# Kernel optimization log

Hardware: AMD Instinct MI355X
Metric: run time of the kernel (lower is better)

Reference implementation:

```python
import jax, jax.numpy as jnp
import numpy as np

E = 8          # moe_num_experts
F = 4096       # ffn_hidden_size
D = 2048       # d_model
TOP_K = 2


def setup_inputs() -> dict:
    key = jax.random.key(0)
    k_x, k_r, k_w1, k_v1, k_w2 = jax.random.split(key, 5)
    scale = 0.02  # ~ normal initializer scale
    x = jax.random.normal(k_x, (2, 2048, D), dtype=jnp.float32)
    router_w = jax.random.normal(k_r, (D, E), dtype=jnp.float32) * scale
    w1 = jax.random.normal(k_w1, (E * F, D), dtype=jnp.float32) * scale
    v1 = jax.random.normal(k_v1, (E * F, D), dtype=jnp.float32) * scale
    w2 = jax.random.normal(k_w2, (E * F, D), dtype=jnp.float32) * scale
    return {"x": x, "router_w": router_w, "w1": w1, "v1": v1, "w2": w2}


def reference(x, router_w, w1, v1, w2):
    # --- Router: dense logits -> softmax (fp32) -> top-k -> L1 normalize ---
    logits = jnp.einsum("bsd,de->bse", x.astype(jnp.float32), router_w)
    weights = jax.nn.softmax(logits, axis=-1)                       # [B,S,E]
    top_weights, top_experts = jax.lax.top_k(weights, TOP_K)        # [B,S,K]
    # moe_normalize_expert_weights = 1 -> L1 norm
    top_weights = top_weights / jnp.sum(jnp.abs(top_weights), axis=-1, keepdims=True)
    top_weights = top_weights.astype(x.dtype)

    # --- Experts: dense per-expert GLU, masked combine (faithful to source) ---
    w1r = w1.reshape(E, F, D)
    v1r = v1.reshape(E, F, D)
    w2r = w2.reshape(E, F, D)
    out = jnp.zeros_like(x)
    for e in range(E):  # fixed small structural loop over experts
        x1 = jnp.einsum("bsd,fd->bsf", x, w1r[e])
        x2 = jnp.einsum("bsd,fd->bsf", x, v1r[e])
        h = jax.nn.silu(x1) * x2                                    # GLU
        y = jnp.einsum("bsf,fd->bsd", h, w2r[e])
        coef = jnp.sum((top_experts == e) * top_weights, axis=-1)[:, :, None]
        out = out + coef * y
    return out
```

## Files before the change

kernel.cpp:

```cpp
#include <hip/hip_runtime.h>
#include <cstdio>
#include <cstdint>

typedef _Float16 f16;
typedef _Float16 f16x8 __attribute__((ext_vector_type(8)));
typedef float f32x4 __attribute__((ext_vector_type(4)));

#define D_MODEL 2048
#define FFN     4096
#define FFN2    8192
#define NEXP    8
#define NTOK    4096
#define NENT    (NTOK*2)
#define BM      256
#define BN      256
#define BK      64
#define KSPLIT  4
#define KCHUNK  (FFN / KSPLIT)
#define MAX_ROWS  10240
#define MAX_TILES 40

__device__ __forceinline__ void gload_lds16(const void* g, void* l) {
  __builtin_amdgcn_global_load_lds(
      (const __attribute__((address_space(1))) void*)g,
      (__attribute__((address_space(3))) void*)l, 16, 0, 0);
}

__device__ __forceinline__ void waitvm0() {
  asm volatile("s_waitcnt vmcnt(0)" ::: "memory");
}

template<int LD>
__device__ __forceinline__ void stageA(const f16* aT, int k0, f16* AS, int mh, int tid) {
#pragma unroll
  for (int s = 0; s < 2; s++) {
    int o = s*8192 + tid*16;
    int rl = o >> 7;
    int ce = ((o & 127) ^ ((rl & 7) << 4)) >> 1;
    int arow = s*128 + mh*64 + (rl & 63);
    gload_lds16(aT + (size_t)arow * LD + k0 + ce,
                (char*)AS + mh*16384 + s*8192 + (tid & ~63)*16);
  }
}

template<int LD>
__device__ __forceinline__ void stageB(const f16* bT, int k0, f16* BS, int nh, int tid) {
#pragma unroll
  for (int s = 0; s < 2; s++) {
    int o = s*8192 + tid*16;
    int rl = o >> 7;
    int ce = ((o & 127) ^ ((rl & 7) << 4)) >> 1;
    int crow = (rl >> 5)*64 + nh*32 + (rl & 31);
    gload_lds16(bT + (size_t)crow * LD + k0 + ce,
                (char*)BS + nh*16384 + s*8192 + (tid & ~63)*16);
  }
}

__device__ __forceinline__ f16x8 fragLd(const f16* S, int row, int lane, int ks) {
  int kb = ks*64 + (lane >> 4)*16;
  int off = (row*128 + kb) ^ ((row & 7) << 4);
  return *(const f16x8*)((const char*)S + off);
}

__device__ __forceinline__ void quad(
    f32x4 (&acc)[8][4], int mo, int no,
    f16x8 (&aF)[4][2], f16x8 (&bFh)[2][2]) {
#pragma unroll
  for (int mf = 0; mf < 4; mf++)
#pragma unroll
    for (int nf = 0; nf < 2; nf++)
#pragma unroll
      for (int ks = 0; ks < 2; ks++)
        acc[mo+mf][no+nf] = __builtin_amdgcn_mfma_f32_16x16x32_f16(
            aF[mf][ks], bFh[nf][ks], acc[mo+mf][no+nf], 0, 0, 0);
}

template<int LD, bool STG>
__device__ __forceinline__ void tileK2(
    const f16* aT, const f16* bT, int k1,
    const f16* ASc, const f16* BSc, f16* ASn, f16* BSn,
    f32x4 (&acc)[8][4], int tid, int lane, int wrM, int wcN) {
  if constexpr (STG) {
    stageA<LD>(aT, k1, ASn, 0, tid);
    stageA<LD>(aT, k1, ASn, 1, tid);
    stageB<LD>(bT, k1, BSn, 0, tid);
    stageB<LD>(bT, k1, BSn, 1, tid);
  }
  f16x8 aF[4][2], bF[2][2][2];
  int i15 = lane & 15;
#pragma unroll
  for (int mf = 0; mf < 4; mf++)
#pragma unroll
    for (int ks = 0; ks < 2; ks++)
      aF[mf][ks] = fragLd(ASc, wrM*64 + mf*16 + i15, lane, ks);
#pragma unroll
  for (int h = 0; h < 2; h++)
#pragma unroll
    for (int nf = 0; nf < 2; nf++)
#pragma unroll
      for (int ks = 0; ks < 2; ks++)
        bF[h][nf][ks] = fragLd(BSc, h*128 + wcN*32 + nf*16 + i15, lane, ks);
  quad(acc, 0, 0, aF, bF[0]);
  quad(acc, 0, 2, aF, bF[1]);
#pragma unroll
  for (int mf = 0; mf < 4; mf++)
#pragma unroll
    for (int ks = 0; ks < 2; ks++)
      aF[mf][ks] = fragLd(ASc, 128 + wrM*64 + mf*16 + i15, lane, ks);
  quad(acc, 4, 0, aF, bF[0]);
  quad(acc, 4, 2, aF, bF[1]);
  if constexpr (STG) waitvm0();
  __builtin_amdgcn_s_barrier();
}


__global__ void zero_counts_kernel(int* counts) {
  if (threadIdx.x < NEXP) counts[threadIdx.x] = 0;
}

__global__ __launch_bounds__(64) void router_kernel(
    const float* __restrict__ x, const float* __restrict__ rw,
    int* counts, int* te, float* tw, int* trank) {
  int t = blockIdx.x;
  int lane = threadIdx.x;
  float acc[8] = {0.f,0.f,0.f,0.f,0.f,0.f,0.f,0.f};
  const float* xr = x + (size_t)t * D_MODEL;
  for (int d = lane; d < D_MODEL; d += 64) {
    float xv = xr[d];
    const float4* r4 = (const float4*)(rw + (size_t)d * NEXP);
    float4 a = r4[0], b = r4[1];
    acc[0] += xv*a.x; acc[1] += xv*a.y; acc[2] += xv*a.z; acc[3] += xv*a.w;
    acc[4] += xv*b.x; acc[5] += xv*b.y; acc[6] += xv*b.z; acc[7] += xv*b.w;
  }
#pragma unroll
  for (int off = 32; off > 0; off >>= 1) {
#pragma unroll
    for (int e = 0; e < 8; e++) acc[e] += __shfl_down(acc[e], off);
  }
  if (lane == 0) {
    int e0 = 0;
#pragma unroll
    for (int e = 1; e < 8; e++) if (acc[e] > acc[e0]) e0 = e;
    int e1 = (e0 == 0) ? 1 : 0;
#pragma unroll
    for (int e = 0; e < 8; e++) if (e != e0 && acc[e] > acc[e1]) e1 = e;
    float c0 = 1.0f / (1.0f + expf(acc[e1] - acc[e0]));
    float c1 = 1.0f - c0;
    int r0 = atomicAdd(&counts[e0], 1);
    int r1 = atomicAdd(&counts[e1], 1);
    te[t*2] = e0; te[t*2+1] = e1;
    tw[t*2] = c0; tw[t*2+1] = c1;
    trank[t*2] = r0; trank[t*2+1] = r1;
  }
}

__global__ void sched_kernel(const int* counts, int* offsets, int4* sched, int* nT) {
  if (threadIdx.x != 0 || blockIdx.x != 0) return;
  int off = 0, n = 0;
  for (int e = 0; e < NEXP; e++) {
    offsets[e] = off;
    int cnt = counts[e];
    int nt = (cnt + BM - 1) / BM;
    for (int i = 0; i < nt; i++) {
      sched[n] = make_int4(e, off + i*BM, min(BM, cnt - i*BM), 0);
      n++;
    }
    off += nt * BM;
  }
  offsets[NEXP] = off;
  *nT = n;
}

__global__ __launch_bounds__(256) void gather_kernel(
    const float* __restrict__ x, const int* __restrict__ te,
    const float* __restrict__ tw, const int* __restrict__ trank,
    const int* __restrict__ offsets, f16* __restrict__ xg,
    int* __restrict__ token_of, float* __restrict__ coefs) {
  int i = blockIdx.x;
  int t = i >> 1;
  int e = te[i];
  int slot = offsets[e] + trank[i];
  if (threadIdx.x == 0) { token_of[slot] = t; coefs[slot] = tw[i]; }
  const float4* src = (const float4*)(x + (size_t)t * D_MODEL);
  f16x8* dst = (f16x8*)(xg + (size_t)slot * D_MODEL);
  for (int j = threadIdx.x; j < D_MODEL/8; j += 256) {
    float4 v0 = src[j*2], v1 = src[j*2+1];
    f16x8 h;
    h[0]=(f16)v0.x; h[1]=(f16)v0.y; h[2]=(f16)v0.z; h[3]=(f16)v0.w;
    h[4]=(f16)v1.x; h[5]=(f16)v1.y; h[6]=(f16)v1.z; h[7]=(f16)v1.w;
    dst[j] = h;
  }
}

__global__ __launch_bounds__(256) void convert_both_kernel(
    const float* __restrict__ w1, const float* __restrict__ v1,
    f16* __restrict__ dst) {
  int n8 = NEXP*FFN*D_MODEL/8;
  int stride = gridDim.x * 256;
  for (int i = blockIdx.x*256 + threadIdx.x; i < n8; i += stride) {
    int d8 = i & (D_MODEL/8 - 1);
    int fr_glob = i >> 8;
    int e = fr_glob >> 12;
    int fr = fr_glob & (FFN - 1);
    int crbase = ((fr >> 4)*2)*16 + (fr & 15);
    float4 a0 = ((const float4*)w1)[(size_t)i*2];
    float4 a1 = ((const float4*)w1)[(size_t)i*2 + 1];
    float4 b0 = ((const float4*)v1)[(size_t)i*2];
    float4 b1 = ((const float4*)v1)[(size_t)i*2 + 1];
    f16x8 ha, hb;
    ha[0]=(f16)a0.x; ha[1]=(f16)a0.y; ha[2]=(f16)a0.z; ha[3]=(f16)a0.w;
    ha[4]=(f16)a1.x; ha[5]=(f16)a1.y; ha[6]=(f16)a1.z; ha[7]=(f16)a1.w;
    hb[0]=(f16)b0.x; hb[1]=(f16)b0.y; hb[2]=(f16)b0.z; hb[3]=(f16)b0.w;
    hb[4]=(f16)b1.x; hb[5]=(f16)b1.y; hb[6]=(f16)b1.z; hb[7]=(f16)b1.w;
    size_t base = ((size_t)e*FFN2 + crbase)*(D_MODEL/8) + d8;
    ((f16x8*)dst)[base] = ha;
    ((f16x8*)dst)[base + 16*(D_MODEL/8)] = hb;
  }
}

__global__ __launch_bounds__(256) void transpose_w2_kernel(
    const float* __restrict__ w2, f16* __restrict__ w2t) {
  __shared__ float tl[64][65];
  int e = blockIdx.z;
  int d0 = blockIdx.x * 64, f0 = blockIdx.y * 64;
  const float* src = w2 + (size_t)e * FFN * D_MODEL;
  int tid = threadIdx.x;
  int fr = tid >> 4, c4 = (tid & 15) * 4;
#pragma unroll
  for (int rr = 0; rr < 4; rr++) {
    float4 v = *(const float4*)(src + (size_t)(f0 + fr + rr*16) * D_MODEL + d0 + c4);
    tl[fr + rr*16][c4+0] = v.x; tl[fr + rr*16][c4+1] = v.y;
    tl[fr + rr*16][c4+2] = v.z; tl[fr + rr*16][c4+3] = v.w;
  }
  __syncthreads();
  int dr = tid >> 2, fg = (tid & 3) * 16;
  f16* dst = w2t + (size_t)e * D_MODEL * FFN + (size_t)(d0 + dr) * FFN + f0 + fg;
  f16 tmp[16];
#pragma unroll
  for (int j = 0; j < 16; j++) tmp[j] = (f16)tl[fg + j][dr];
  *(float4*)(dst)     = *(float4*)(tmp);
  *(float4*)(dst + 8) = *(float4*)(tmp + 8);
}

__global__ __launch_bounds__(512, 2) void phaseA_kernel(
    const f16* __restrict__ xg, const f16* __restrict__ w12h,
    f16* __restrict__ hbuf, const int4* __restrict__ sched, const int* __restrict__ nT) {
  int tile = blockIdx.y;
  if (tile >= *nT) return;
  int4 sc = sched[tile];
  int e = sc.x, row0 = sc.y;
  int fc0 = blockIdx.x * BN;

  __shared__ f16 AS[2][BM*BK];
  __shared__ f16 BS[2][BN*BK];

  int tid = threadIdx.x, lane = tid & 63, wid = tid >> 6;
  int wrM = wid >> 2, wcN = wid & 3;

  const f16* aT = xg  + (size_t)row0 * D_MODEL;
  const f16* bT = w12h + (size_t)e * FFN2 * D_MODEL + (size_t)fc0 * D_MODEL;

  f32x4 acc[8][4];
  f32x4 z4 = {0.f,0.f,0.f,0.f};
#pragma unroll
  for (int m = 0; m < 8; m++)
#pragma unroll
    for (int n = 0; n < 4; n++) acc[m][n] = z4;

  stageA<D_MODEL>(aT, 0, AS[0], 0, tid);
  stageA<D_MODEL>(aT, 0, AS[0], 1, tid);
  stageB<D_MODEL>(bT, 0, BS[0], 0, tid);
  stageB<D_MODEL>(bT, 0, BS[0], 1, tid);
  waitvm0();
  __builtin_amdgcn_s_barrier();

  constexpr int NTILES = D_MODEL / BK;
  for (int t = 0; t < NTILES - 1; t++) {
    int b = t & 1;
    tileK2<D_MODEL,true>(aT, bT, (t+1)*BK, AS[b], BS[b], AS[b^1], BS[b^1],
                         acc, tid, lane, wrM, wcN);
  }
  tileK2<D_MODEL,false>(aT, bT, 0, AS[(NTILES-1)&1], BS[(NTILES-1)&1],
                        AS[NTILES&1], BS[NTILES&1], acc, tid, lane, wrM, wcN);

  int i15 = lane & 15, l4 = lane >> 4;
#pragma unroll
  for (int m = 0; m < 8; m++) {
    int rowl = wrM*128 + (m>>2)*64 + (m&3)*16 + l4*4;
#pragma unroll
    for (int nh = 0; nh < 2; nh++) {
      int f = (fc0 >> 1) + wcN*32 + nh*16 + i15;
      f16* hb = hbuf + (size_t)(row0 + rowl) * FFN + f;
#pragma unroll
      for (int q2 = 0; q2 < 4; q2++) {
        float x1 = acc[m][nh*2+0][q2], x2 = acc[m][nh*2+1][q2];
        float hv = x1 / (1.0f + __expf(-x1)) * x2;
        hb[(size_t)q2 * FFN] = (f16)hv;
      }
    }
  }
}

__global__ __launch_bounds__(512, 2) void phaseB_kernel(
    const f16* __restrict__ hbuf, const f16* __restrict__ w2t,
    f16* __restrict__ yb0, f16* __restrict__ ybR,
    const int4* __restrict__ sched, const int* __restrict__ nT) {
  int tile = blockIdx.y;
  if (tile >= *nT) return;
  int4 sc = sched[tile];
  int e = sc.x, row0 = sc.y;
  int dc0 = blockIdx.x * BN;
  int z = blockIdx.z;

  __shared__ f16 AS[2][BM*BK];
  __shared__ f16 BS[2][BN*BK];

  int tid = threadIdx.x, lane = tid & 63, wid = tid >> 6;
  int wrM = wid >> 2, wcN = wid & 3;

  const f16* aT = hbuf + (size_t)row0 * FFN + z * KCHUNK;
  const f16* bT = w2t + (size_t)e * D_MODEL * FFN + (size_t)dc0 * FFN + z * KCHUNK;

  f32x4 acc[8][4];
  f32x4 z4 = {0.f,0.f,0.f,0.f};
#pragma unroll
  for (int m = 0; m < 8; m++)
#pragma unroll
    for (int n = 0; n < 4; n++) acc[m][n] = z4;

  stageA<FFN>(aT, 0, AS[0], 0, tid);
  stageA<FFN>(aT, 0, AS[0], 1, tid);
  stageB<FFN>(bT, 0, BS[0], 0, tid);
  stageB<FFN>(bT, 0, BS[0], 1, tid);
  waitvm0();
  __builtin_amdgcn_s_barrier();

  constexpr int NTILES = KCHUNK / BK;
  for (int t = 0; t < NTILES - 1; t++) {
    int b = t & 1;
    tileK2<FFN,true>(aT, bT, (t+1)*BK, AS[b], BS[b], AS[b^1], BS[b^1],
                     acc, tid, lane, wrM, wcN);
  }
  tileK2<FFN,false>(aT, bT, 0, AS[(NTILES-1)&1], BS[(NTILES-1)&1],
                    AS[NTILES&1], BS[NTILES&1], acc, tid, lane, wrM, wcN);

  f16* yb = (z == 0) ? yb0 : (ybR + (size_t)(z-1) * MAX_ROWS * D_MODEL);
  int i15 = lane & 15, l4 = lane >> 4;
#pragma unroll
  for (int m = 0; m < 8; m++) {
#pragma unroll
    for (int q2 = 0; q2 < 4; q2++) {
      int rl = wrM*128 + (m>>2)*64 + (m&3)*16 + l4*4 + q2;
      f16* yrow = yb + (size_t)(row0 + rl) * D_MODEL + dc0 + wcN*64;
#pragma unroll
      for (int n = 0; n < 4; n++)
        yrow[(n>>1)*32 + (n&1)*16 + i15] = (f16)acc[m][n][q2];
    }
  }
}

__global__ __launch_bounds__(256) void combine_kernel(
    const f16* __restrict__ yb0, const f16* __restrict__ ybR,
    const int* __restrict__ te, const float* __restrict__ tw,
    const int* __restrict__ trank, const int* __restrict__ offsets,
    float* __restrict__ out) {
  int t = blockIdx.x;
  int d8 = threadIdx.x;
  int s0 = offsets[te[2*t]]   + trank[2*t];
  int s1 = offsets[te[2*t+1]] + trank[2*t+1];
  float w0 = tw[2*t], w1 = tw[2*t+1];
  float sum[8] = {0.f,0.f,0.f,0.f,0.f,0.f,0.f,0.f};
#pragma unroll
  for (int z = 0; z < KSPLIT; z++) {
    const f16* yb = (z == 0) ? yb0 : (ybR + (size_t)(z-1) * MAX_ROWS * D_MODEL);
    f16x8 a = ((const f16x8*)(yb + (size_t)s0 * D_MODEL))[d8];
    f16x8 b = ((const f16x8*)(yb + (size_t)s1 * D_MODEL))[d8];
#pragma unroll
    for (int j = 0; j < 8; j++) sum[j] += w0 * (float)a[j] + w1 * (float)b[j];
  }
  float* o = out + (size_t)t * D_MODEL + d8*8;
  float4 o0 = {sum[0], sum[1], sum[2], sum[3]};
  float4 o1 = {sum[4], sum[5], sum[6], sum[7]};
  ((float4*)o)[0] = o0;
  ((float4*)o)[1] = o1;
}

extern "C" void kernel_launch(void* const* d_in, const int* in_sizes, int n_in,
                              void* d_out, int out_size, void* d_ws, size_t ws_size,
                              hipStream_t stream) {
  const float* x  = (const float*)d_in[0];
  const float* rw = (const float*)d_in[1];
  const float* w1 = (const float*)d_in[2];
  const float* v1 = (const float*)d_in[3];
  const float* w2 = (const float*)d_in[4];
  float* out = (float*)d_out;

  char* p = (char*)d_ws;
  auto alloc = [&](size_t bytes) {
    char* r = p;
    p += (bytes + 255) & ~(size_t)255;
    return r;
  };
  int*   counts   = (int*)  alloc(NEXP * 4);
  int*   nT       = (int*)  alloc(4);
  int*   offsets  = (int*)  alloc((NEXP + 1) * 4);
  int*   te       = (int*)  alloc(NENT * 4);
  float* tw       = (float*)alloc(NENT * 4);
  int*   trank    = (int*)  alloc(NENT * 4);
  int*   token_of = (int*)  alloc(MAX_ROWS * 4);
  float* coefs    = (float*)alloc(MAX_ROWS * 4);
  int4*  sched    = (int4*) alloc(MAX_TILES * 16);
  f16*   xg       = (f16*)  alloc((size_t)MAX_ROWS * D_MODEL * 2);
  f16*   hbuf     = (f16*)  alloc((size_t)MAX_ROWS * FFN * 2);
  f16*   w12h     = (f16*)  alloc((size_t)NEXP * FFN2 * D_MODEL * 2);
  f16*   w2t      = (f16*)  alloc((size_t)NEXP * FFN * D_MODEL * 2);
  size_t needed = (size_t)(p - (char*)d_ws);
  if (needed > ws_size) {
    fprintf(stderr, "kernel_launch: ws too small: need %zu, have %zu\n", needed, ws_size);
    return;
  }
  f16* yb0 = xg;
  f16* ybR = w12h;

  zero_counts_kernel<<<1, 64, 0, stream>>>(counts);
  router_kernel<<<NTOK, 64, 0, stream>>>(x, rw, counts, te, tw, trank);
  sched_kernel<<<1, 1, 0, stream>>>(counts, offsets, sched, nT);
  gather_kernel<<<NENT, 256, 0, stream>>>(x, te, tw, trank, offsets, xg, token_of, coefs);
  convert_both_kernel<<<4096, 256, 0, stream>>>(w1, v1, w12h);
  transpose_w2_kernel<<<dim3(D_MODEL/64, FFN/64, NEXP), 256, 0, stream>>>(w2, w2t);
  phaseA_kernel<<<dim3(FFN2/BN, MAX_TILES), 512, 0, stream>>>(xg, w12h, hbuf, sched, nT);
  phaseB_kernel<<<dim3(D_MODEL/BN, MAX_TILES, KSPLIT), 512, 0, stream>>>(hbuf, w2t, yb0, ybR, sched, nT);
  combine_kernel<<<NTOK, 256, 0, stream>>>(yb0, ybR, te, tw, trank, offsets, out);
}
```

Baseline: 1.009 ms.

## Prefetch two K-tiles ahead with split-phase loads interleaved between MFMA quads

```diff
diff --git a/kernel.cpp b/kernel.cpp
--- a/kernel.cpp
+++ b/kernel.cpp
@@ -26,8 +26,9 @@
       (__attribute__((address_space(3))) void*)l, 16, 0, 0);
 }
 
-__device__ __forceinline__ void waitvm0() {
-  asm volatile("s_waitcnt vmcnt(0)" ::: "memory");
+template<int N> __device__ __forceinline__ void waitvm() {
+  if constexpr (N == 0) asm volatile("s_waitcnt vmcnt(0)" ::: "memory");
+  else if constexpr (N == 8) asm volatile("s_waitcnt vmcnt(8)" ::: "memory");
 }
 
 template<int LD>
@@ -64,7 +65,7 @@
 
 __device__ __forceinline__ void quad(
     f32x4 (&acc)[8][4], int mo, int no,
-    f16x8 (&aF)[4][2], f16x8 (&bFh)[2][2]) {
+    f16x8 (&aFh)[4][2], f16x8 (&bFh)[2][2]) {
 #pragma unroll
   for (int mf = 0; mf < 4; mf++)
 #pragma unroll
@@ -72,44 +73,65 @@
 #pragma unroll
       for (int ks = 0; ks < 2; ks++)
         acc[mo+mf][no+nf] = __builtin_amdgcn_mfma_f32_16x16x32_f16(
-            aF[mf][ks], bFh[nf][ks], acc[mo+mf][no+nf], 0, 0, 0);
-}
-
-template<int LD, bool STG>
-__device__ __forceinline__ void tileK2(
-    const f16* aT, const f16* bT, int k1,
-    const f16* ASc, const f16* BSc, f16* ASn, f16* BSn,
-    f32x4 (&acc)[8][4], int tid, int lane, int wrM, int wcN) {
+            aFh[mf][ks], bFh[nf][ks], acc[mo+mf][no+nf], 0, 0, 0);
+}
+
+template<int LD, int VEND, bool STG>
+__device__ __forceinline__ void tile4v2(
+    const f16* aT, const f16* bT, int k2,
+    f16* ASc, f16* BSc,
+    f32x4 (&acc)[8][4],
+    int tid, int lane, int wrM, int wcN) {
+  f16x8 aF0[4][2], aF1[4][2], bF[2][2][2];
+  int i15 = lane & 15;
+#pragma unroll
+  for (int mf = 0; mf < 4; mf++)
+#pragma unroll
+    for (int ks = 0; ks < 2; ks++)
+      aF0[mf][ks] = fragLd(ASc, wrM*64 + mf*16 + i15, lane, ks);
+#pragma unroll
+  for (int nf = 0; nf < 2; nf++)
+#pragma unroll
+    for (int ks = 0; ks < 2; ks++)
+      bF[0][nf][ks] = fragLd(BSc, wcN*32 + nf*16 + i15, lane, ks);
+  __builtin_amdgcn_s_barrier();
+  __builtin_amdgcn_s_setprio(1);
+  quad(acc, 0, 0, aF0, bF[0]);
+  __builtin_amdgcn_s_setprio(0);
+  __builtin_amdgcn_s_barrier();
+#pragma unroll
+  for (int nf = 0; nf < 2; nf++)
+#pragma unroll
+    for (int ks = 0; ks < 2; ks++)
+      bF[1][nf][ks] = fragLd(BSc, 128 + wcN*32 + nf*16 + i15, lane, ks);
+#pragma unroll
+  for (int mf = 0; mf < 4; mf++)
+#pragma unroll
+    for (int ks = 0; ks < 2; ks++)
+      aF1[mf][ks] = fragLd(ASc, 128 + wrM*64 + mf*16 + i15, lane, ks);
+  __builtin_amdgcn_s_barrier();
+  __builtin_amdgcn_s_setprio(1);
+  quad(acc, 0, 2, aF0, bF[1]);
+  __builtin_amdgcn_s_setprio(0);
+  __builtin_amdgcn_s_barrier();
   if constexpr (STG) {
-    stageA<LD>(aT, k1, ASn, 0, tid);
-    stageA<LD>(aT, k1, ASn, 1, tid);
-    stageB<LD>(bT, k1, BSn, 0, tid);
-    stageB<LD>(bT, k1, BSn, 1, tid);
-  }
-  f16x8 aF[4][2], bF[2][2][2];
-  int i15 = lane & 15;
-#pragma unroll
-  for (int mf = 0; mf < 4; mf++)
-#pragma unroll
-    for (int ks = 0; ks < 2; ks++)
-      aF[mf][ks] = fragLd(ASc, wrM*64 + mf*16 + i15, lane, ks);
-#pragma unroll
-  for (int h = 0; h < 2; h++)
-#pragma unroll
-    for (int nf = 0; nf < 2; nf++)
-#pragma unroll
-      for (int ks = 0; ks < 2; ks++)
-        bF[h][nf][ks] = fragLd(BSc, h*128 + wcN*32 + nf*16 + i15, lane, ks);
-  quad(acc, 0, 0, aF, bF[0]);
-  quad(acc, 0, 2, aF, bF[1]);
-#pragma unroll
-  for (int mf = 0; mf < 4; mf++)
-#pragma unroll
-    for (int ks = 0; ks < 2; ks++)
-      aF[mf][ks] = fragLd(ASc, 128 + wrM*64 + mf*16 + i15, lane, ks);
-  quad(acc, 4, 0, aF, bF[0]);
-  quad(acc, 4, 2, aF, bF[1]);
-  if constexpr (STG) waitvm0();
+    stageB<LD>(bT, k2, BSc, 0, tid);
+    stageB<LD>(bT, k2, BSc, 1, tid);
+  }
+  __builtin_amdgcn_s_barrier();
+  __builtin_amdgcn_s_setprio(1);
+  quad(acc, 4, 0, aF1, bF[0]);
+  __builtin_amdgcn_s_setprio(0);
+  __builtin_amdgcn_s_barrier();
+  if constexpr (STG) {
+    stageA<LD>(aT, k2, ASc, 0, tid);
+    stageA<LD>(aT, k2, ASc, 1, tid);
+  }
+  __builtin_amdgcn_s_barrier();
+  __builtin_amdgcn_s_setprio(1);
+  quad(acc, 4, 2, aF1, bF[1]);
+  __builtin_amdgcn_s_setprio(0);
+  waitvm<VEND>();
   __builtin_amdgcn_s_barrier();
 }
 
@@ -271,17 +293,23 @@
   stageA<D_MODEL>(aT, 0, AS[0], 1, tid);
   stageB<D_MODEL>(bT, 0, BS[0], 0, tid);
   stageB<D_MODEL>(bT, 0, BS[0], 1, tid);
-  waitvm0();
+  stageA<D_MODEL>(aT, BK, AS[1], 0, tid);
+  stageA<D_MODEL>(aT, BK, AS[1], 1, tid);
+  stageB<D_MODEL>(bT, BK, BS[1], 0, tid);
+  stageB<D_MODEL>(bT, BK, BS[1], 1, tid);
+  waitvm<8>();
   __builtin_amdgcn_s_barrier();
 
   constexpr int NTILES = D_MODEL / BK;
-  for (int t = 0; t < NTILES - 1; t++) {
+  for (int t = 0; t + 2 < NTILES; t++) {
     int b = t & 1;
-    tileK2<D_MODEL,true>(aT, bT, (t+1)*BK, AS[b], BS[b], AS[b^1], BS[b^1],
-                         acc, tid, lane, wrM, wcN);
-  }
-  tileK2<D_MODEL,false>(aT, bT, 0, AS[(NTILES-1)&1], BS[(NTILES-1)&1],
-                        AS[NTILES&1], BS[NTILES&1], acc, tid, lane, wrM, wcN);
+    tile4v2<D_MODEL,8,true>(aT, bT, (t+2)*BK, AS[b], BS[b],
+                            acc, tid, lane, wrM, wcN);
+  }
+  tile4v2<D_MODEL,0,false>(aT, bT, 0, AS[(NTILES-2)&1], BS[(NTILES-2)&1],
+                           acc, tid, lane, wrM, wcN);
+  tile4v2<D_MODEL,-1,false>(aT, bT, 0, AS[(NTILES-1)&1], BS[(NTILES-1)&1],
+                            acc, tid, lane, wrM, wcN);
 
   int i15 = lane & 15, l4 = lane >> 4;
 #pragma unroll
@@ -332,17 +360,23 @@
   stageA<FFN>(aT, 0, AS[0], 1, tid);
   stageB<FFN>(bT, 0, BS[0], 0, tid);
   stageB<FFN>(bT, 0, BS[0], 1, tid);
-  waitvm0();
+  stageA<FFN>(aT, BK, AS[1], 0, tid);
+  stageA<FFN>(aT, BK, AS[1], 1, tid);
+  stageB<FFN>(bT, BK, BS[1], 0, tid);
+  stageB<FFN>(bT, BK, BS[1], 1, tid);
+  waitvm<8>();
   __builtin_amdgcn_s_barrier();
 
   constexpr int NTILES = KCHUNK / BK;
-  for (int t = 0; t < NTILES - 1; t++) {
+  for (int t = 0; t + 2 < NTILES; t++) {
     int b = t & 1;
-    tileK2<FFN,true>(aT, bT, (t+1)*BK, AS[b], BS[b], AS[b^1], BS[b^1],
-                     acc, tid, lane, wrM, wcN);
-  }
-  tileK2<FFN,false>(aT, bT, 0, AS[(NTILES-1)&1], BS[(NTILES-1)&1],
-                    AS[NTILES&1], BS[NTILES&1], acc, tid, lane, wrM, wcN);
+    tile4v2<FFN,8,true>(aT, bT, (t+2)*BK, AS[b], BS[b],
+                        acc, tid, lane, wrM, wcN);
+  }
+  tile4v2<FFN,0,false>(aT, bT, 0, AS[(NTILES-2)&1], BS[(NTILES-2)&1],
+                       acc, tid, lane, wrM, wcN);
+  tile4v2<FFN,-1,false>(aT, bT, 0, AS[(NTILES-1)&1], BS[(NTILES-1)&1],
+                        acc, tid, lane, wrM, wcN);
 
   f16* yb = (z == 0) ? yb0 : (ybR + (size_t)(z-1) * MAX_ROWS * D_MODEL);
   int i15 = lane & 15, l4 = lane >> 4;
```

After: 1.053 ms. +4.3%, slower.
